# Performance work log

Measured on AMD Instinct MI355X. Metric: run time of the kernel, lower is better.

Reference implementation:

```python
import jax, jax.numpy as jnp
import numpy as np

NUM_HEADS = 16
NEG_INF = -1000000.0  # matches torch masked_fill value


def setup_inputs() -> dict:
    key = jax.random.key(0)
    k1, k2, k3, k4, k5, k6 = jax.random.split(key, 6)
    N, S, E = 2, 2048, 1024
    x_encoder = jax.random.normal(k1, (N, S, E), dtype=jnp.float32)
    x_decoder = jax.random.normal(k2, (N, S, E), dtype=jnp.float32)
    mask = jax.random.randint(k3, (S, S), 0, 2, dtype=jnp.int32)
    W_qk = jax.random.normal(k4, (2 * E, E), dtype=jnp.float32) * (1.0 / np.sqrt(E))
    W_v = jax.random.normal(k5, (E, E), dtype=jnp.float32) * (1.0 / np.sqrt(E))
    W_o = jax.random.normal(k6, (E, E), dtype=jnp.float32) * (1.0 / np.sqrt(E))
    return {"x_encoder": x_encoder, "x_decoder": x_decoder, "mask": mask,
            "W_qk": W_qk, "W_v": W_v, "W_o": W_o}


def reference(x_encoder, x_decoder, mask, W_qk, W_v, W_o):
    N, S, E = x_encoder.shape
    H = NUM_HEADS
    hd = E // H
    # projections (no bias)
    qk = x_encoder @ W_qk.T            # (N, S, 2E)
    v = x_decoder @ W_v.T              # (N, S, E)
    qk = qk.reshape(N, S, H, 2 * hd).transpose(0, 2, 1, 3)  # (N, H, S, 2hd)
    v = v.reshape(N, S, H, hd).transpose(0, 2, 1, 3)         # (N, H, S, hd)
    q, k = qk[..., :hd], qk[..., hd:]
    # scaled dot-product attention with mask fill
    logits = jnp.einsum('bhqd,bhkd->bhqk', q, k) / jnp.sqrt(jnp.float32(hd))
    m = mask[None, None, :, :]  # expand_mask: 2D -> (1,1,S,S)
    logits = jnp.where(m == 0, jnp.float32(NEG_INF), logits)
    attn = jax.nn.softmax(logits, axis=-1)
    vals = jnp.einsum('bhqk,bhkd->bhqd', attn, v)            # (N, H, S, hd)
    vals = vals.transpose(0, 2, 1, 3).reshape(N, S, E)
    return vals @ W_o.T
```

## Files before the change

### kernel.cpp

```cpp
#include <hip/hip_runtime.h>

typedef __attribute__((ext_vector_type(8))) short short8;
typedef __attribute__((ext_vector_type(4))) float f32x4;
typedef __attribute__((ext_vector_type(4))) unsigned short u16x4;
typedef __attribute__((ext_vector_type(4))) unsigned int u32x4;

#define MFMA16(A,B,C) __builtin_amdgcn_mfma_f32_16x16x32_bf16(A,B,C,0,0,0)

__device__ __forceinline__ unsigned short f2bf(float f) {
  unsigned int u = __builtin_bit_cast(unsigned int, f);
  unsigned int r = (u + 0x7fffu + ((u >> 16) & 1u)) >> 16;
  return (unsigned short)r;
}

__device__ __forceinline__ unsigned int cvt_pk_bf16(float lo, float hi) {
  unsigned int r;
  asm("v_cvt_pk_bf16_f32 %0, %1, %2" : "=v"(r) : "v"(lo), "v"(hi));
  return r;
}

__device__ __forceinline__ f32x4 zero4() {
  f32x4 z; z.x = 0.f; z.y = 0.f; z.z = 0.f; z.w = 0.f; return z;
}

__device__ __forceinline__ void gl_lds16(const void* g, void* l) {
  __builtin_amdgcn_global_load_lds((const __attribute__((address_space(1))) void*)g,
                                   (__attribute__((address_space(3))) void*)l, 16, 0, 0);
}

__global__ __launch_bounds__(256) void cvt_all(const float* __restrict__ xe,
                                               const float* __restrict__ xd,
                                               const float* __restrict__ wqk,
                                               const float* __restrict__ wv,
                                               const float* __restrict__ wo,
                                               unsigned short* __restrict__ ws) {
  long i = (long)blockIdx.x * 256 + threadIdx.x;
  const float* src; unsigned short* dst; long o;
  if (i < 1048576)      { src = xe;  dst = ws + 8650752;  o = i; }
  else if (i < 2097152) { src = xd;  dst = ws + 12845056; o = i - 1048576; }
  else if (i < 2621440) { src = wqk; dst = ws + 17039360; o = i - 2097152; }
  else if (i < 2883584) { src = wv;  dst = ws + 19136512; o = i - 2621440; }
  else                  { src = wo;  dst = ws + 20185088; o = i - 2883584; }
  float4 f = ((const float4*)src)[o];
  u16x4 r; r.x = f2bf(f.x); r.y = f2bf(f.y); r.z = f2bf(f.z); r.w = f2bf(f.w);
  ((u16x4*)dst)[o] = r;
}

__global__ __launch_bounds__(256) void mask_pack(const int* __restrict__ mask,
                                                 unsigned int* __restrict__ mbits) {
  int idx = blockIdx.x * 256 + threadIdx.x;
  int row = idx >> 6, wi = idx & 63;
  const int* p = mask + (long)row * 2048 + wi * 32;
  unsigned int bits = 0;
  #pragma unroll
  for (int j = 0; j < 32; j++) bits |= (p[j] != 0 ? 1u : 0u) << j;
  mbits[idx] = bits;
}

template <int MODE>
__global__ __launch_bounds__(256) void gemm_bt(const unsigned short* __restrict__ A,
                                               const unsigned short* __restrict__ B,
                                               void* __restrict__ Cv,
                                               int M, int N, int K) {
  __shared__ __align__(16) unsigned short As[128 * 64];
  __shared__ __align__(16) unsigned short Bs[128 * 64];
  const int tid = threadIdx.x;
  const int w = tid >> 6, l = tid & 63;
  const int wr = w >> 1, wc = w & 1;
  const long row0 = (long)blockIdx.y * 128;
  const long col0 = (long)blockIdx.x * 128;
  const int lr = l >> 3;
  const int lc = (l & 7) * 8;

  f32x4 acc[4][4];
  #pragma unroll
  for (int m = 0; m < 4; m++)
    #pragma unroll
    for (int n = 0; n < 4; n++) acc[m][n] = zero4();

  for (int k0 = 0; k0 < K; k0 += 64) {
    #pragma unroll
    for (int j = 0; j < 4; j++) {
      int slot = j * 4 + w;
      int row = slot * 8 + lr;
      gl_lds16(A + (row0 + row) * K + k0 + lc, &As[slot * 512]);
      gl_lds16(B + (col0 + row) * K + k0 + lc, &Bs[slot * 512]);
    }
    __syncthreads();
    #pragma unroll
    for (int kk = 0; kk < 2; kk++) {
      short8 a[4], b[4];
      #pragma unroll
      for (int m = 0; m < 4; m++)
        a[m] = *(const short8*)&As[(wr * 64 + m * 16 + (l & 15)) * 64 + kk * 32 + (l >> 4) * 8];
      #pragma unroll
      for (int n = 0; n < 4; n++)
        b[n] = *(const short8*)&Bs[(wc * 64 + n * 16 + (l & 15)) * 64 + kk * 32 + (l >> 4) * 8];
      #pragma unroll
      for (int m = 0; m < 4; m++)
        #pragma unroll
        for (int n = 0; n < 4; n++)
          acc[m][n] = MFMA16(a[m], b[n], acc[m][n]);
    }
    __syncthreads();
  }

  #pragma unroll
  for (int m = 0; m < 4; m++) {
    long rowb = row0 + wr * 64 + m * 16 + ((l >> 4) * 4);
    #pragma unroll
    for (int n = 0; n < 4; n++) {
      long colb = col0 + wc * 64 + n * 16 + (l & 15);
      if (MODE == 0) {
        unsigned short* C = (unsigned short*)Cv;
        #pragma unroll
        for (int r = 0; r < 4; r++) C[(rowb + r) * N + colb] = f2bf(acc[m][n][r]);
      } else if (MODE == 1) {
        unsigned short* C = (unsigned short*)Cv;
        long bb = rowb >> 11, s0 = rowb & 2047;
        u16x4 pk;
        pk.x = f2bf(acc[m][n][0]); pk.y = f2bf(acc[m][n][1]);
        pk.z = f2bf(acc[m][n][2]); pk.w = f2bf(acc[m][n][3]);
        *(u16x4*)&C[(bb * 1024 + colb) * 2048 + s0] = pk;
      } else {
        float* C = (float*)Cv;
        #pragma unroll
        for (int r = 0; r < 4; r++) C[(rowb + r) * N + colb] = acc[m][n][r];
      }
    }
  }
}

__device__ __forceinline__ void softmax_pack(const f32x4* sf, unsigned long long mw,
                                             int g, int sA, int sB, int gh, float SC,
                                             float& l_run, short8& pa0o, short8& pa1o) {
  mw >>= (g * 4);
  unsigned int mlo = (unsigned int)mw, mhi = (unsigned int)(mw >> 32);
  float pv[16];
  float lsum = 0.f;
  #pragma unroll
  for (int kvq = 0; kvq < 4; kvq++) {
    unsigned int msel = (kvq < 2) ? mlo : mhi;
    #pragma unroll
    for (int r = 0; r < 4; r++) {
      float e = __builtin_amdgcn_exp2f(sf[kvq][r] * SC);
      unsigned int bit = (msel >> (((kvq & 1) << 4) + r)) & 1u;
      float p = bit ? e : 0.0f;
      pv[kvq * 4 + r] = p;
      lsum += p;
    }
  }
  l_run += lsum;

  unsigned int pk0[2], pk1[2], pk2[2], pk3[2];
  pk0[0] = cvt_pk_bf16(pv[0],  pv[1]);  pk0[1] = cvt_pk_bf16(pv[2],  pv[3]);
  pk1[0] = cvt_pk_bf16(pv[4],  pv[5]);  pk1[1] = cvt_pk_bf16(pv[6],  pv[7]);
  pk2[0] = cvt_pk_bf16(pv[8],  pv[9]);  pk2[1] = cvt_pk_bf16(pv[10], pv[11]);
  pk3[0] = cvt_pk_bf16(pv[12], pv[13]); pk3[1] = cvt_pk_bf16(pv[14], pv[15]);

  u32x4 a0, a1;
  int t0, t1;
  t0 = __shfl((int)pk0[0], sA); t1 = __shfl((int)pk1[0], sA);
  a0.x = gh ? (unsigned)t1 : (unsigned)t0;
  t0 = __shfl((int)pk0[1], sA); t1 = __shfl((int)pk1[1], sA);
  a0.y = gh ? (unsigned)t1 : (unsigned)t0;
  t0 = __shfl((int)pk0[0], sB); t1 = __shfl((int)pk1[0], sB);
  a0.z = gh ? (unsigned)t1 : (unsigned)t0;
  t0 = __shfl((int)pk0[1], sB); t1 = __shfl((int)pk1[1], sB);
  a0.w = gh ? (unsigned)t1 : (unsigned)t0;
  t0 = __shfl((int)pk2[0], sA); t1 = __shfl((int)pk3[0], sA);
  a1.x = gh ? (unsigned)t1 : (unsigned)t0;
  t0 = __shfl((int)pk2[1], sA); t1 = __shfl((int)pk3[1], sA);
  a1.y = gh ? (unsigned)t1 : (unsigned)t0;
  t0 = __shfl((int)pk2[0], sB); t1 = __shfl((int)pk3[0], sB);
  a1.z = gh ? (unsigned)t1 : (unsigned)t0;
  t0 = __shfl((int)pk2[1], sB); t1 = __shfl((int)pk3[1], sB);
  a1.w = gh ? (unsigned)t1 : (unsigned)t0;
  pa0o = __builtin_bit_cast(short8, a0);
  pa1o = __builtin_bit_cast(short8, a1);
}

__global__ __launch_bounds__(256, 4) void attn(const unsigned short* __restrict__ qk,
                                               const unsigned short* __restrict__ vT,
                                               const unsigned int* __restrict__ mbits,
                                               unsigned short* __restrict__ po0,
                                               unsigned short* __restrict__ po1,
                                               float* __restrict__ pl0,
                                               float* __restrict__ pl1) {
  __shared__ __align__(16) unsigned short Ks[2][64 * 64];
  const int tid = threadIdx.x;
  const int w = tid >> 6, l = tid & 63;
  const int b = blockIdx.z, h = blockIdx.y;
  const int qt = blockIdx.x & 15, kvh = blockIdx.x >> 4;
  const int q0 = qt * 128;
  const int kvbase = kvh << 10;
  unsigned short* po = kvh ? po1 : po0;
  float* pl = kvh ? pl1 : pl0;
  const int c = l & 15, g = l >> 4;
  const int lr = l >> 3, pg = l & 7;

  const int qa = q0 + w * 32 + c;
  const int qb = qa + 16;
  const unsigned short* qptrA = qk + (long)(b * 2048 + qa) * 2048 + h * 128;
  const unsigned short* qptrB = qk + (long)(b * 2048 + qb) * 2048 + h * 128;
  short8 bqA0 = *(const short8*)&qptrA[g * 8];
  short8 bqA1 = *(const short8*)&qptrA[32 + g * 8];
  short8 bqB0 = *(const short8*)&qptrB[g * 8];
  short8 bqB1 = *(const short8*)&qptrB[32 + g * 8];

  const float SC = 0.125f * 1.4426950408889634f;
  const int sw0 = ((g)     ^ (c & 7)) * 8;
  const int sw1 = ((g + 4) ^ (c & 7)) * 8;
  const int sA = c + (((2 * g)     & 3) << 4);
  const int sB = c + (((2 * g + 1) & 3) << 4);
  const int gh = g >> 1;

  const unsigned int* mrowA = mbits + (long)qa * 64;
  const unsigned int* mrowB = mbits + (long)qb * 64;

  const unsigned short* kbase = qk + (long)b * 2048 * 2048 + h * 128 + 64;
  const unsigned short* vbase = vT + (long)((b * 16 + h) * 64) * 2048;
  const int srow = w * 8 + lr;
  const int sgg = pg ^ (lr & 7);

  float lA = 0.f, lB = 0.f;
  f32x4 oA[4], oB[4];
  #pragma unroll
  for (int d = 0; d < 4; d++) { oA[d] = zero4(); oB[d] = zero4(); }

  #pragma unroll
  for (int j = 0; j < 2; j++) {
    int row = srow + j * 32;
    gl_lds16(kbase + (long)(kvbase + row) * 2048 + sgg * 8, &Ks[0][(w + j * 4) * 512]);
  }
  __syncthreads();

  for (int it = 0; it < 16; it++) {
    const int kv0 = kvbase + it * 64;
    const int cur = it & 1;

    if (it < 15) {
      #pragma unroll
      for (int j = 0; j < 2; j++) {
        int row = srow + j * 32;
        gl_lds16(kbase + (long)(kv0 + 64 + row) * 2048 + sgg * 8,
                 &Ks[cur ^ 1][(w + j * 4) * 512]);
      }
    }

    short8 vf[8];
    #pragma unroll
    for (int dt = 0; dt < 4; dt++) {
      const unsigned short* vp = vbase + (long)(dt * 16 + c) * 2048 + kv0;
      vf[dt * 2]     = *(const short8*)&vp[g * 8];
      vf[dt * 2 + 1] = *(const short8*)&vp[32 + g * 8];
    }
    unsigned long long mwA = *(const unsigned long long*)&mrowA[kv0 >> 5];
    unsigned long long mwB = *(const unsigned long long*)&mrowB[kv0 >> 5];

    f32x4 sfA[4], sfB[4];
    #pragma unroll
    for (int kvq = 0; kvq < 4; kvq++) {
      int R = kvq * 16 + c;
      short8 ak0 = *(const short8*)&Ks[cur][R * 64 + sw0];
      short8 ak1 = *(const short8*)&Ks[cur][R * 64 + sw1];
      f32x4 zA = zero4();
      zA = MFMA16(ak0, bqA0, zA);
      zA = MFMA16(ak1, bqA1, zA);
      sfA[kvq] = zA;
      f32x4 zB = zero4();
      zB = MFMA16(ak0, bqB0, zB);
      zB = MFMA16(ak1, bqB1, zB);
      sfB[kvq] = zB;
    }

    short8 paA0, paA1, paB0, paB1;
    softmax_pack(sfA, mwA, g, sA, sB, gh, SC, lA, paA0, paA1);
    softmax_pack(sfB, mwB, g, sA, sB, gh, SC, lB, paB0, paB1);

    #pragma unroll
    for (int dt = 0; dt < 4; dt++) {
      oA[dt] = MFMA16(paA0, vf[dt * 2],     oA[dt]);
      oA[dt] = MFMA16(paA1, vf[dt * 2 + 1], oA[dt]);
      oB[dt] = MFMA16(paB0, vf[dt * 2],     oB[dt]);
      oB[dt] = MFMA16(paB1, vf[dt * 2 + 1], oB[dt]);
    }

    __syncthreads();
  }

  lA += __shfl_xor(lA, 16); lA += __shfl_xor(lA, 32);
  lB += __shfl_xor(lB, 16); lB += __shfl_xor(lB, 32);
  if (g == 0) {
    pl[((long)(b << 11) + qa) * 16 + h] = lA;
    pl[((long)(b << 11) + qb) * 16 + h] = lB;
  }
  #pragma unroll
  for (int dt = 0; dt < 4; dt++) {
    long rowA = (long)b * 2048 + q0 + w * 32 + g * 4;
    long rowB = rowA + 16;
    int col = h * 64 + dt * 16 + c;
    po[(rowA + 0) * 1024 + col] = f2bf(oA[dt][0]);
    po[(rowA + 1) * 1024 + col] = f2bf(oA[dt][1]);
    po[(rowA + 2) * 1024 + col] = f2bf(oA[dt][2]);
    po[(rowA + 3) * 1024 + col] = f2bf(oA[dt][3]);
    po[(rowB + 0) * 1024 + col] = f2bf(oB[dt][0]);
    po[(rowB + 1) * 1024 + col] = f2bf(oB[dt][1]);
    po[(rowB + 2) * 1024 + col] = f2bf(oB[dt][2]);
    po[(rowB + 3) * 1024 + col] = f2bf(oB[dt][3]);
  }
}

__global__ __launch_bounds__(256) void combine(const unsigned short* __restrict__ po0,
                                               const unsigned short* __restrict__ po1,
                                               const float* __restrict__ pl0,
                                               const float* __restrict__ pl1,
                                               unsigned short* __restrict__ vals) {
  int i = blockIdx.x * 256 + threadIdx.x;
  int q = i >> 7;
  int col = (i & 127) * 8;
  int h = col >> 6;
  float linv = 1.0f / (pl0[q * 16 + h] + pl1[q * 16 + h]);
  long off = (long)q * 1024 + col;
  short8 a = *(const short8*)&po0[off];
  short8 b = *(const short8*)&po1[off];
  short8 o;
  #pragma unroll
  for (int j = 0; j < 8; j++) {
    float fa = __builtin_bit_cast(float, ((unsigned int)(unsigned short)a[j]) << 16);
    float fb = __builtin_bit_cast(float, ((unsigned int)(unsigned short)b[j]) << 16);
    o[j] = (short)f2bf((fa + fb) * linv);
  }
  *(short8*)&vals[off] = o;
}

extern "C" void kernel_launch(void* const* d_in, const int* in_sizes, int n_in,
                              void* d_out, int out_size, void* d_ws, size_t ws_size,
                              hipStream_t stream) {
  const float* xe  = (const float*)d_in[0];
  const float* xd  = (const float*)d_in[1];
  const int*   msk = (const int*)d_in[2];
  const float* wqk = (const float*)d_in[3];
  const float* wv  = (const float*)d_in[4];
  const float* wo  = (const float*)d_in[5];
  float* out = (float*)d_out;
  unsigned short* ws = (unsigned short*)d_ws;

  unsigned short* po0    = ws;
  unsigned short* po1    = ws + 4194304;
  float*          pl0    = (float*)(ws + 8388608);
  float*          pl1    = (float*)(ws + 8519680);
  unsigned short* xe_bf  = ws + 8650752;
  unsigned short* xd_bf  = ws + 12845056;
  unsigned short* wqk_bf = ws + 17039360;
  unsigned short* wv_bf  = ws + 19136512;
  unsigned short* wo_bf  = ws + 20185088;
  unsigned short* qkb    = ws + 21233664;
  unsigned short* vTb    = ws + 29622272;
  unsigned short* valb   = ws + 33816576;
  unsigned int*   mbits  = (unsigned int*)(ws + 38010880);

  cvt_all<<<12288, 256, 0, stream>>>(xe, xd, wqk, wv, wo, ws);
  mask_pack<<<512, 256, 0, stream>>>(msk, mbits);
  gemm_bt<0><<<dim3(16, 32), 256, 0, stream>>>(xe_bf, wqk_bf, qkb, 4096, 2048, 1024);
  gemm_bt<1><<<dim3(8, 32), 256, 0, stream>>>(xd_bf, wv_bf, vTb, 4096, 1024, 1024);
  attn<<<dim3(32, 16, 2), 256, 0, stream>>>(qkb, vTb, mbits, po0, po1, pl0, pl1);
  combine<<<2048, 256, 0, stream>>>(po0, po1, pl0, pl1, valb);
  gemm_bt<2><<<dim3(8, 32), 256, 0, stream>>>(valb, wo_bf, out, 4096, 1024, 1024);
}
```

Baseline: 188.6 us.

## Fold softmax scale into W_q conversion and halve attention query tile

```diff
diff --git a/kernel.cpp b/kernel.cpp
--- a/kernel.cpp
+++ b/kernel.cpp
@@ -35,13 +35,18 @@
                                                const float* __restrict__ wo,
                                                unsigned short* __restrict__ ws) {
   long i = (long)blockIdx.x * 256 + threadIdx.x;
-  const float* src; unsigned short* dst; long o;
+  const float* src; unsigned short* dst; long o; bool scl = false;
   if (i < 1048576)      { src = xe;  dst = ws + 8650752;  o = i; }
   else if (i < 2097152) { src = xd;  dst = ws + 12845056; o = i - 1048576; }
-  else if (i < 2621440) { src = wqk; dst = ws + 17039360; o = i - 2097152; }
+  else if (i < 2621440) { src = wqk; dst = ws + 17039360; o = i - 2097152;
+                          scl = (((o >> 8) & 127) < 64); }
   else if (i < 2883584) { src = wv;  dst = ws + 19136512; o = i - 2621440; }
   else                  { src = wo;  dst = ws + 20185088; o = i - 2883584; }
   float4 f = ((const float4*)src)[o];
+  if (scl) {
+    const float SCQ = 0.125f * 1.4426950408889634f;
+    f.x *= SCQ; f.y *= SCQ; f.z *= SCQ; f.w *= SCQ;
+  }
   u16x4 r; r.x = f2bf(f.x); r.y = f2bf(f.y); r.z = f2bf(f.z); r.w = f2bf(f.w);
   ((u16x4*)dst)[o] = r;
 }
@@ -132,7 +137,7 @@
 }
 
 __device__ __forceinline__ void softmax_pack(const f32x4* sf, unsigned long long mw,
-                                             int g, int sA, int sB, int gh, float SC,
+                                             int g, int sA, int sB, int gh,
                                              float& l_run, short8& pa0o, short8& pa1o) {
   mw >>= (g * 4);
   unsigned int mlo = (unsigned int)mw, mhi = (unsigned int)(mw >> 32);
@@ -143,7 +148,7 @@
     unsigned int msel = (kvq < 2) ? mlo : mhi;
     #pragma unroll
     for (int r = 0; r < 4; r++) {
-      float e = __builtin_amdgcn_exp2f(sf[kvq][r] * SC);
+      float e = __builtin_amdgcn_exp2f(sf[kvq][r]);
       unsigned int bit = (msel >> (((kvq & 1) << 4) + r)) & 1u;
       float p = bit ? e : 0.0f;
       pv[kvq * 4 + r] = p;
@@ -191,48 +196,41 @@
   const int tid = threadIdx.x;
   const int w = tid >> 6, l = tid & 63;
   const int b = blockIdx.z, h = blockIdx.y;
-  const int qt = blockIdx.x & 15, kvh = blockIdx.x >> 4;
-  const int q0 = qt * 128;
+  const int qt = blockIdx.x & 31, kvh = blockIdx.x >> 5;
+  const int q0 = qt * 64;
   const int kvbase = kvh << 10;
   unsigned short* po = kvh ? po1 : po0;
   float* pl = kvh ? pl1 : pl0;
   const int c = l & 15, g = l >> 4;
   const int lr = l >> 3, pg = l & 7;
 
-  const int qa = q0 + w * 32 + c;
-  const int qb = qa + 16;
-  const unsigned short* qptrA = qk + (long)(b * 2048 + qa) * 2048 + h * 128;
-  const unsigned short* qptrB = qk + (long)(b * 2048 + qb) * 2048 + h * 128;
-  short8 bqA0 = *(const short8*)&qptrA[g * 8];
-  short8 bqA1 = *(const short8*)&qptrA[32 + g * 8];
-  short8 bqB0 = *(const short8*)&qptrB[g * 8];
-  short8 bqB1 = *(const short8*)&qptrB[32 + g * 8];
-
-  const float SC = 0.125f * 1.4426950408889634f;
+  const int qrow = q0 + w * 16 + c;
+  const unsigned short* qptr = qk + (long)(b * 2048 + qrow) * 2048 + h * 128;
+  short8 bq0 = *(const short8*)&qptr[g * 8];
+  short8 bq1 = *(const short8*)&qptr[32 + g * 8];
+
   const int sw0 = ((g)     ^ (c & 7)) * 8;
   const int sw1 = ((g + 4) ^ (c & 7)) * 8;
   const int sA = c + (((2 * g)     & 3) << 4);
   const int sB = c + (((2 * g + 1) & 3) << 4);
   const int gh = g >> 1;
 
-  const unsigned int* mrowA = mbits + (long)qa * 64;
-  const unsigned int* mrowB = mbits + (long)qb * 64;
+  const unsigned int* mrowp = mbits + (long)qrow * 64;
 
   const unsigned short* kbase = qk + (long)b * 2048 * 2048 + h * 128 + 64;
   const unsigned short* vbase = vT + (long)((b * 16 + h) * 64) * 2048;
   const int srow = w * 8 + lr;
   const int sgg = pg ^ (lr & 7);
 
-  float lA = 0.f, lB = 0.f;
-  f32x4 oA[4], oB[4];
-  #pragma unroll
-  for (int d = 0; d < 4; d++) { oA[d] = zero4(); oB[d] = zero4(); }
-
-  #pragma unroll
-  for (int j = 0; j < 2; j++) {
-    int row = srow + j * 32;
-    gl_lds16(kbase + (long)(kvbase + row) * 2048 + sgg * 8, &Ks[0][(w + j * 4) * 512]);
-  }
+  float l_run = 0.f;
+  f32x4 o[4];
+  #pragma unroll
+  for (int d = 0; d < 4; d++) o[d] = zero4();
+
+  #pragma unroll
+  for (int j = 0; j < 2; j++)
+    gl_lds16(kbase + (long)(kvbase + srow + j * 32) * 2048 + sgg * 8,
+             &Ks[0][(w + j * 4) * 512]);
   __syncthreads();
 
   for (int it = 0; it < 16; it++) {
@@ -241,11 +239,9 @@
 
     if (it < 15) {
       #pragma unroll
-      for (int j = 0; j < 2; j++) {
-        int row = srow + j * 32;
-        gl_lds16(kbase + (long)(kv0 + 64 + row) * 2048 + sgg * 8,
+      for (int j = 0; j < 2; j++)
+        gl_lds16(kbase + (long)(kv0 + 64 + srow + j * 32) * 2048 + sgg * 8,
                  &Ks[cur ^ 1][(w + j * 4) * 512]);
-      }
     }
 
     short8 vf[8];
@@ -255,59 +251,43 @@
       vf[dt * 2]     = *(const short8*)&vp[g * 8];
       vf[dt * 2 + 1] = *(const short8*)&vp[32 + g * 8];
     }
-    unsigned long long mwA = *(const unsigned long long*)&mrowA[kv0 >> 5];
-    unsigned long long mwB = *(const unsigned long long*)&mrowB[kv0 >> 5];
-
-    f32x4 sfA[4], sfB[4];
+    unsigned long long mw = *(const unsigned long long*)&mrowp[kv0 >> 5];
+
+    f32x4 sf[4];
     #pragma unroll
     for (int kvq = 0; kvq < 4; kvq++) {
       int R = kvq * 16 + c;
       short8 ak0 = *(const short8*)&Ks[cur][R * 64 + sw0];
       short8 ak1 = *(const short8*)&Ks[cur][R * 64 + sw1];
-      f32x4 zA = zero4();
-      zA = MFMA16(ak0, bqA0, zA);
-      zA = MFMA16(ak1, bqA1, zA);
-      sfA[kvq] = zA;
-      f32x4 zB = zero4();
-      zB = MFMA16(ak0, bqB0, zB);
-      zB = MFMA16(ak1, bqB1, zB);
-      sfB[kvq] = zB;
-    }
-
-    short8 paA0, paA1, paB0, paB1;
-    softmax_pack(sfA, mwA, g, sA, sB, gh, SC, lA, paA0, paA1);
-    softmax_pack(sfB, mwB, g, sA, sB, gh, SC, lB, paB0, paB1);
+      f32x4 z = zero4();
+      z = MFMA16(ak0, bq0, z);
+      z = MFMA16(ak1, bq1, z);
+      sf[kvq] = z;
+    }
+
+    short8 pa0, pa1;
+    softmax_pack(sf, mw, g, sA, sB, gh, l_run, pa0, pa1);
 
     #pragma unroll
     for (int dt = 0; dt < 4; dt++) {
-      oA[dt] = MFMA16(paA0, vf[dt * 2],     oA[dt]);
-      oA[dt] = MFMA16(paA1, vf[dt * 2 + 1], oA[dt]);
-      oB[dt] = MFMA16(paB0, vf[dt * 2],     oB[dt]);
-      oB[dt] = MFMA16(paB1, vf[dt * 2 + 1], oB[dt]);
+      o[dt] = MFMA16(pa0, vf[dt * 2],     o[dt]);
+      o[dt] = MFMA16(pa1, vf[dt * 2 + 1], o[dt]);
     }
 
     __syncthreads();
   }
 
-  lA += __shfl_xor(lA, 16); lA += __shfl_xor(lA, 32);
-  lB += __shfl_xor(lB, 16); lB += __shfl_xor(lB, 32);
-  if (g == 0) {
-    pl[((long)(b << 11) + qa) * 16 + h] = lA;
-    pl[((long)(b << 11) + qb) * 16 + h] = lB;
-  }
+  l_run += __shfl_xor(l_run, 16);
+  l_run += __shfl_xor(l_run, 32);
+  if (g == 0) pl[((long)(b << 11) + qrow) * 16 + h] = l_run;
   #pragma unroll
   for (int dt = 0; dt < 4; dt++) {
-    long rowA = (long)b * 2048 + q0 + w * 32 + g * 4;
-    long rowB = rowA + 16;
+    long rowb = (long)b * 2048 + q0 + w * 16 + g * 4;
     int col = h * 64 + dt * 16 + c;
-    po[(rowA + 0) * 1024 + col] = f2bf(oA[dt][0]);
-    po[(rowA + 1) * 1024 + col] = f2bf(oA[dt][1]);
-    po[(rowA + 2) * 1024 + col] = f2bf(oA[dt][2]);
-    po[(rowA + 3) * 1024 + col] = f2bf(oA[dt][3]);
-    po[(rowB + 0) * 1024 + col] = f2bf(oB[dt][0]);
-    po[(rowB + 1) * 1024 + col] = f2bf(oB[dt][1]);
-    po[(rowB + 2) * 1024 + col] = f2bf(oB[dt][2]);
-    po[(rowB + 3) * 1024 + col] = f2bf(oB[dt][3]);
+    po[(rowb + 0) * 1024 + col] = f2bf(o[dt][0]);
+    po[(rowb + 1) * 1024 + col] = f2bf(o[dt][1]);
+    po[(rowb + 2) * 1024 + col] = f2bf(o[dt][2]);
+    po[(rowb + 3) * 1024 + col] = f2bf(o[dt][3]);
   }
 }
 
@@ -364,7 +344,7 @@
   mask_pack<<<512, 256, 0, stream>>>(msk, mbits);
   gemm_bt<0><<<dim3(16, 32), 256, 0, stream>>>(xe_bf, wqk_bf, qkb, 4096, 2048, 1024);
   gemm_bt<1><<<dim3(8, 32), 256, 0, stream>>>(xd_bf, wv_bf, vTb, 4096, 1024, 1024);
-  attn<<<dim3(32, 16, 2), 256, 0, stream>>>(qkb, vTb, mbits, po0, po1, pl0, pl1);
+  attn<<<dim3(64, 16, 2), 256, 0, stream>>>(qkb, vTb, mbits, po0, po1, pl0, pl1);
   combine<<<2048, 256, 0, stream>>>(po0, po1, pl0, pl1, valb);
   gemm_bt<2><<<dim3(8, 32), 256, 0, stream>>>(valb, wo_bf, out, 4096, 1024, 1024);
 }
```

Result: slower. 243.5 us (+29.1%).

## Stage V tiles through LDS with async loads and fold softmax scale into W_q

Applied to the files above, without the earlier changes.

```diff
diff --git a/kernel.cpp b/kernel.cpp
--- a/kernel.cpp
+++ b/kernel.cpp
@@ -35,13 +35,18 @@
                                                const float* __restrict__ wo,
                                                unsigned short* __restrict__ ws) {
   long i = (long)blockIdx.x * 256 + threadIdx.x;
-  const float* src; unsigned short* dst; long o;
+  const float* src; unsigned short* dst; long o; bool scl = false;
   if (i < 1048576)      { src = xe;  dst = ws + 8650752;  o = i; }
   else if (i < 2097152) { src = xd;  dst = ws + 12845056; o = i - 1048576; }
-  else if (i < 2621440) { src = wqk; dst = ws + 17039360; o = i - 2097152; }
+  else if (i < 2621440) { src = wqk; dst = ws + 17039360; o = i - 2097152;
+                          scl = (((o >> 8) & 127) < 64); }
   else if (i < 2883584) { src = wv;  dst = ws + 19136512; o = i - 2621440; }
   else                  { src = wo;  dst = ws + 20185088; o = i - 2883584; }
   float4 f = ((const float4*)src)[o];
+  if (scl) {
+    const float SCQ = 0.125f * 1.4426950408889634f;
+    f.x *= SCQ; f.y *= SCQ; f.z *= SCQ; f.w *= SCQ;
+  }
   u16x4 r; r.x = f2bf(f.x); r.y = f2bf(f.y); r.z = f2bf(f.z); r.w = f2bf(f.w);
   ((u16x4*)dst)[o] = r;
 }
@@ -132,7 +137,7 @@
 }
 
 __device__ __forceinline__ void softmax_pack(const f32x4* sf, unsigned long long mw,
-                                             int g, int sA, int sB, int gh, float SC,
+                                             int g, int sA, int sB, int gh,
                                              float& l_run, short8& pa0o, short8& pa1o) {
   mw >>= (g * 4);
   unsigned int mlo = (unsigned int)mw, mhi = (unsigned int)(mw >> 32);
@@ -143,7 +148,7 @@
     unsigned int msel = (kvq < 2) ? mlo : mhi;
     #pragma unroll
     for (int r = 0; r < 4; r++) {
-      float e = __builtin_amdgcn_exp2f(sf[kvq][r] * SC);
+      float e = __builtin_amdgcn_exp2f(sf[kvq][r]);
       unsigned int bit = (msel >> (((kvq & 1) << 4) + r)) & 1u;
       float p = bit ? e : 0.0f;
       pv[kvq * 4 + r] = p;
@@ -188,6 +193,7 @@
                                                float* __restrict__ pl0,
                                                float* __restrict__ pl1) {
   __shared__ __align__(16) unsigned short Ks[2][64 * 64];
+  __shared__ __align__(16) unsigned short Vs[2][64 * 64];
   const int tid = threadIdx.x;
   const int w = tid >> 6, l = tid & 63;
   const int b = blockIdx.z, h = blockIdx.y;
@@ -208,7 +214,6 @@
   short8 bqB0 = *(const short8*)&qptrB[g * 8];
   short8 bqB1 = *(const short8*)&qptrB[32 + g * 8];
 
-  const float SC = 0.125f * 1.4426950408889634f;
   const int sw0 = ((g)     ^ (c & 7)) * 8;
   const int sw1 = ((g + 4) ^ (c & 7)) * 8;
   const int sA = c + (((2 * g)     & 3) << 4);
@@ -232,6 +237,7 @@
   for (int j = 0; j < 2; j++) {
     int row = srow + j * 32;
     gl_lds16(kbase + (long)(kvbase + row) * 2048 + sgg * 8, &Ks[0][(w + j * 4) * 512]);
+    gl_lds16(vbase + (long)row * 2048 + kvbase + sgg * 8,   &Vs[0][(w + j * 4) * 512]);
   }
   __syncthreads();
 
@@ -245,16 +251,11 @@
         int row = srow + j * 32;
         gl_lds16(kbase + (long)(kv0 + 64 + row) * 2048 + sgg * 8,
                  &Ks[cur ^ 1][(w + j * 4) * 512]);
+        gl_lds16(vbase + (long)row * 2048 + kv0 + 64 + sgg * 8,
+                 &Vs[cur ^ 1][(w + j * 4) * 512]);
       }
     }
 
-    short8 vf[8];
-    #pragma unroll
-    for (int dt = 0; dt < 4; dt++) {
-      const unsigned short* vp = vbase + (long)(dt * 16 + c) * 2048 + kv0;
-      vf[dt * 2]     = *(const short8*)&vp[g * 8];
-      vf[dt * 2 + 1] = *(const short8*)&vp[32 + g * 8];
-    }
     unsigned long long mwA = *(const unsigned long long*)&mrowA[kv0 >> 5];
     unsigned long long mwB = *(const unsigned long long*)&mrowB[kv0 >> 5];
 
@@ -275,15 +276,18 @@
     }
 
     short8 paA0, paA1, paB0, paB1;
-    softmax_pack(sfA, mwA, g, sA, sB, gh, SC, lA, paA0, paA1);
-    softmax_pack(sfB, mwB, g, sA, sB, gh, SC, lB, paB0, paB1);
+    softmax_pack(sfA, mwA, g, sA, sB, gh, lA, paA0, paA1);
+    softmax_pack(sfB, mwB, g, sA, sB, gh, lB, paB0, paB1);
 
     #pragma unroll
     for (int dt = 0; dt < 4; dt++) {
-      oA[dt] = MFMA16(paA0, vf[dt * 2],     oA[dt]);
-      oA[dt] = MFMA16(paA1, vf[dt * 2 + 1], oA[dt]);
-      oB[dt] = MFMA16(paB0, vf[dt * 2],     oB[dt]);
-      oB[dt] = MFMA16(paB1, vf[dt * 2 + 1], oB[dt]);
+      int d = dt * 16 + c;
+      short8 bv0 = *(const short8*)&Vs[cur][d * 64 + sw0];
+      short8 bv1 = *(const short8*)&Vs[cur][d * 64 + sw1];
+      oA[dt] = MFMA16(paA0, bv0, oA[dt]);
+      oA[dt] = MFMA16(paA1, bv1, oA[dt]);
+      oB[dt] = MFMA16(paB0, bv0, oB[dt]);
+      oB[dt] = MFMA16(paB1, bv1, oB[dt]);
     }
 
     __syncthreads();
```

Result: faster. 167.6 us (-11.1%).
